# Kernel tuning notes

Measured on AMD Instinct MI355X. Metric: run time of the kernel, lower is better.

## Reference

```python
import jax
import jax.numpy as jnp
import numpy as np
from jax import lax

DIM = 48
HIDDEN = int(DIM * 2.66)  # 127, matches torch int(dim*ffn_expansion_factor)
EPS_LN = 1e-5
EPS_NORM = 1e-12


def conv2d(x, w, groups=1):
    # x: NCHW, w: OIHW, stride 1, SAME padding (all kernels here are 1x1 or 3x3 pad=1)
    return lax.conv_general_dilated(
        x, w, window_strides=(1, 1), padding='SAME',
        feature_group_count=groups,
        dimension_numbers=('NCHW', 'OIHW', 'NCHW'))


def layernorm_cbias(x, w, b):
    # Restormer WithBias_LayerNorm: normalize over channel dim (biased var)
    mu = jnp.mean(x, axis=1, keepdims=True)
    var = jnp.mean(jnp.square(x - mu), axis=1, keepdims=True)
    xn = (x - mu) * lax.rsqrt(var + EPS_LN)
    return xn * w[None, :, None, None] + b[None, :, None, None]


def l2norm_last(x):
    # torch F.normalize(dim=-1, eps=1e-12)
    n = jnp.sqrt(jnp.sum(jnp.square(x), axis=-1, keepdims=True))
    return x / jnp.maximum(n, EPS_NORM)


def setup_inputs() -> dict:
    key = jax.random.key(0)
    ks = jax.random.split(key, 16)
    s = 0.05
    B, H, W = 2, 512, 512
    return {
        'x': jax.random.normal(ks[0], (B, 3, H, W), dtype=jnp.float32),
        # OverlapPatchEmbed: Conv2d(3, 48, 3, pad=1, bias=False)
        'pe_w': jax.random.normal(ks[1], (DIM, 3, 3, 3), dtype=jnp.float32) * s,
        # norm1 (WithBias)
        'n1_w': jnp.ones((DIM,), dtype=jnp.float32),
        'n1_b': jnp.zeros((DIM,), dtype=jnp.float32),
        # MDTA attention, num_heads=1
        'temp': jnp.ones((1, 1, 1), dtype=jnp.float32),
        'qkv_w': jax.random.normal(ks[2], (DIM * 3, DIM, 1, 1), dtype=jnp.float32) * s,
        'qkv_dw_w': jax.random.normal(ks[3], (DIM * 3, 1, 3, 3), dtype=jnp.float32) * s,
        'po_w': jax.random.normal(ks[4], (DIM, DIM, 1, 1), dtype=jnp.float32) * s,
        # norm2
        'n2_w': jnp.ones((DIM,), dtype=jnp.float32),
        'n2_b': jnp.zeros((DIM,), dtype=jnp.float32),
        # GDFN
        'pi_w': jax.random.normal(ks[5], (HIDDEN * 2, DIM, 1, 1), dtype=jnp.float32) * s,
        'ffn_dw_w': jax.random.normal(ks[6], (HIDDEN * 2, 1, 3, 3), dtype=jnp.float32) * s,
        'fo_w': jax.random.normal(ks[7], (DIM, HIDDEN, 1, 1), dtype=jnp.float32) * s,
    }


def reference(x, pe_w, n1_w, n1_b, temp, qkv_w, qkv_dw_w, po_w, n2_w, n2_b, pi_w, ffn_dw_w, fo_w):
    # Patch embed
    patch = conv2d(x, pe_w)  # [B, 48, H, W]
    B, C, H, W = patch.shape

    # ---- MDTA channel attention on norm1(patch) ----
    y = layernorm_cbias(patch, n1_w, n1_b)
    qkv = conv2d(conv2d(y, qkv_w), qkv_dw_w, groups=3 * C)  # [B, 3C, H, W]
    q, k, v = jnp.split(qkv, 3, axis=1)
    # heads=1: rearrange to [B, C, H*W]
    q = l2norm_last(q.reshape(B, C, H * W))
    k = l2norm_last(k.reshape(B, C, H * W))
    v = v.reshape(B, C, H * W)
    attn = jax.nn.softmax(jnp.einsum('bcn,bdn->bcd', q, k) * temp[0, 0, 0], axis=-1)  # [B, C, C]
    out = jnp.einsum('bcd,bdn->bcn', attn, v).reshape(B, C, H, W)
    attn_out = conv2d(out, po_w)
    first = patch + attn_out

    # ---- GDFN on norm2(first) ----
    y2 = layernorm_cbias(first, n2_w, n2_b)
    h = conv2d(conv2d(y2, pi_w), ffn_dw_w, groups=2 * HIDDEN)  # [B, 254, H, W]
    x1, x2 = jnp.split(h, 2, axis=1)
    ffn = conv2d(jax.nn.gelu(x1, approximate=False) * x2, fo_w)
    return first + ffn  # second_residual [B, 48, H, W]
```

## Files before the change

### kernel.cpp

```cpp
#include <hip/hip_runtime.h>
#include <hip/hip_bf16.h>
#include <math.h>

#define HW 512
#define NPIX (HW*HW)

typedef __hip_bfloat16 bf16;
typedef __attribute__((ext_vector_type(8))) unsigned short u16x8;
typedef __attribute__((ext_vector_type(8))) short s16x8;
typedef __attribute__((ext_vector_type(4))) float f32x4;

__device__ __forceinline__ float b2f(bf16 v) { return __bfloat162float(v); }
__device__ __forceinline__ bf16 f2b(float v) { return __float2bfloat16(v); }

union fu { float f; unsigned int u; };
union bu { bf16 b; unsigned short u; };

__device__ __forceinline__ float us2f(unsigned short u) {
    fu c; c.u = ((unsigned int)u) << 16; return c.f;
}

__device__ __forceinline__ void ld_bf8(const bf16* p, float* f) {
    u16x8 u = *(const u16x8*)p;
#pragma unroll
    for (int j = 0; j < 8; j++) { fu c; c.u = ((unsigned int)u[j]) << 16; f[j] = c.f; }
}

__device__ __forceinline__ void st_bf8(bf16* p, const float* f) {
    u16x8 u;
#pragma unroll
    for (int j = 0; j < 8; j++) { bu c; c.b = f2b(f[j]); u[j] = c.u; }
    *(u16x8*)p = u;
}

__global__ __launch_bounds__(256) void k_prep(const float* __restrict__ qkvw,
                                              const float* __restrict__ piw,
                                              const float* __restrict__ fow,
                                              bf16* __restrict__ WQ,
                                              bf16* __restrict__ WP,
                                              bf16* __restrict__ WF,
                                              float* __restrict__ Z0,
                                              float* __restrict__ Z1)
{
    int idx = blockIdx.x*256 + threadIdx.x;
    if (idx < 9216) {
        int oc = idx >> 6, k = idx & 63;
        WQ[idx] = f2b(k < 48 ? qkvw[oc*48 + k] : 0.f);
    } else if (idx < 25600) {
        int j = idx - 9216; int oc = j >> 6, k = j & 63;
        WP[j] = f2b((oc < 254 && k < 48) ? piw[oc*48 + k] : 0.f);
    } else if (idx < 31744) {
        int j = idx - 25600; int oc = j >> 7, k = j & 127;
        WF[j] = f2b(k < 127 ? fow[oc*127 + k] : 0.f);
    } else if (idx < 36544) {
        int j = idx - 31744;
        if (j < 2400) Z0[j] = 0.f; else Z1[j-2400] = 0.f;
    }
}

__global__ __launch_bounds__(256) void k_pe(const float* __restrict__ x,
                                            const float* __restrict__ w,
                                            bf16* __restrict__ out)
{
    __shared__ float ws[48*27];
    for (int i = threadIdx.x; i < 48*27; i += 256) ws[i] = w[i];
    __syncthreads();
    int lane = threadIdx.x & 63, wv = threadIdx.x >> 6;
    int row = blockIdx.x*4 + wv;
    int col = lane*8;
    float a[3][3][8];
    float lf[3][3], rt[3][3];
#pragma unroll
    for (int c = 0; c < 3; c++)
#pragma unroll
        for (int r = 0; r < 3; r++) {
            int rr = row + r - 1;
            if (rr >= 0 && rr < HW) {
                const float* p = x + (size_t)c*NPIX + rr*HW + col;
                float4 u0 = *(const float4*)p, u1 = *(const float4*)(p+4);
                a[c][r][0]=u0.x; a[c][r][1]=u0.y; a[c][r][2]=u0.z; a[c][r][3]=u0.w;
                a[c][r][4]=u1.x; a[c][r][5]=u1.y; a[c][r][6]=u1.z; a[c][r][7]=u1.w;
            } else {
#pragma unroll
                for (int j = 0; j < 8; j++) a[c][r][j] = 0.f;
            }
            float l = __shfl_up(a[c][r][7], 1);  lf[c][r] = (lane==0)  ? 0.f : l;
            float rv= __shfl_down(a[c][r][0],1); rt[c][r] = (lane==63) ? 0.f : rv;
        }
    for (int oc = 0; oc < 48; oc++) {
        float acc[8];
#pragma unroll
        for (int j = 0; j < 8; j++) acc[j] = 0.f;
#pragma unroll
        for (int c = 0; c < 3; c++)
#pragma unroll
            for (int r = 0; r < 3; r++) {
                float w0 = ws[oc*27 + c*9 + r*3 + 0];
                float w1 = ws[oc*27 + c*9 + r*3 + 1];
                float w2 = ws[oc*27 + c*9 + r*3 + 2];
#pragma unroll
                for (int j = 0; j < 8; j++) {
                    float xm = (j==0) ? lf[c][r] : a[c][r][j-1];
                    float x0 = a[c][r][j];
                    float xp = (j==7) ? rt[c][r] : a[c][r][j+1];
                    acc[j] += w0*xm + w1*x0 + w2*xp;
                }
            }
        st_bf8(out + (size_t)oc*NPIX + row*HW + col, acc);
    }
}

#define YPAD 56
#define CHS 440
__global__ __launch_bounds__(256) void k_ln_dw(const bf16* __restrict__ patch,
                                               const float* __restrict__ lnw,
                                               const float* __restrict__ lnb,
                                               const s16x8* __restrict__ wq,
                                               const float* __restrict__ dww,
                                               bf16* __restrict__ outq)
{
    __shared__ unsigned short y_lds[352*YPAD];
    __shared__ unsigned short a_lds[48*CHS];
    int t = threadIdx.x;
    int c0 = blockIdx.x*32, r0 = blockIdx.y*8;

    for (int hp = t; hp < 352; hp += 256) {
        int hr = hp/34, hc = hp - hr*34;
        int gr = r0 - 1 + hr, gc = c0 - 1 + hc;
        bool ok = (hp < 340) && (gr >= 0) && (gr < HW) && (gc >= 0) && (gc < HW);
        if (ok) {
            int gpx = gr*HW + gc;
            float y[48];
            float mu = 0.f;
#pragma unroll
            for (int i = 0; i < 48; i++) { y[i] = b2f(patch[(size_t)i*NPIX + gpx]); mu += y[i]; }
            mu *= (1.f/48.f);
            float var = 0.f;
#pragma unroll
            for (int i = 0; i < 48; i++) { float d = y[i]-mu; var += d*d; }
            float s = rsqrtf(var*(1.f/48.f) + 1e-5f);
#pragma unroll
            for (int i = 0; i < 48; i++) y[i] = (y[i]-mu)*s*lnw[i] + lnb[i];
#pragma unroll
            for (int kb = 0; kb < 6; kb++) {
                union { u16x8 v; unsigned short us[8]; } pk;
#pragma unroll
                for (int j = 0; j < 8; j++) { bu b; b.b = f2b(y[kb*8+j]); pk.us[j] = b.u; }
                *(u16x8*)&y_lds[hp*YPAD + kb*8] = pk.v;
            }
        } else {
            u16x8 z = {0,0,0,0,0,0,0,0};
#pragma unroll
            for (int kb = 0; kb < 6; kb++) *(u16x8*)&y_lds[hp*YPAD + kb*8] = z;
        }
    }
    __syncthreads();

    int lane = t & 63, wv = t >> 6;
    int q = lane >> 4, n = lane & 15;
    int ch2 = lane >> 5;
    int idx5 = lane & 31;
    int orow = idx5 >> 2;
    int cg   = idx5 & 3;

#pragma unroll 1
    for (int cc = 0; cc < 3; cc++) {
        s16x8 a0[3], a1[3];
#pragma unroll
        for (int mi = 0; mi < 3; mi++) {
            int oc = (cc*3 + mi)*16 + n;
            a0[mi] = wq[oc*8 + q];
            a1[mi] = wq[oc*8 + 4 + q];
        }
#pragma unroll 1
        for (int nt = wv; nt < 22; nt += 4) {
            int hp = nt*16 + n;
            int hr = hp/34, hc = hp - hr*34;
            int abase = hr*40 + hc;
            s16x8 b0 = *(const s16x8*)&y_lds[hp*YPAD + q*8];
            s16x8 b1 = {0,0,0,0,0,0,0,0};
            if (q < 2) b1 = *(const s16x8*)&y_lds[hp*YPAD + 32 + q*8];
#pragma unroll
            for (int mi = 0; mi < 3; mi++) {
                f32x4 acc = {0.f, 0.f, 0.f, 0.f};
                acc = __builtin_amdgcn_mfma_f32_16x16x32_bf16(a0[mi], b0, acc, 0, 0, 0);
                acc = __builtin_amdgcn_mfma_f32_16x16x32_bf16(a1[mi], b1, acc, 0, 0, 0);
                int mchb = mi*16 + q*4;
#pragma unroll
                for (int r = 0; r < 4; r++) {
                    bu bb; bb.b = f2b(acc[r]);
                    a_lds[(mchb + r)*CHS + abase] = bb.u;
                }
            }
        }
        __syncthreads();

#pragma unroll 1
        for (int i = 0; i < 6; i++) {
            int chl = i*8 + wv*2 + ch2;
            int ch  = cc*48 + chl;
            float wk[9];
#pragma unroll
            for (int k = 0; k < 9; k++) wk[k] = dww[ch*9 + k];
            const unsigned short* ap = &a_lds[chl*CHS];
            float win[3][10];
#pragma unroll
            for (int kr = 0; kr < 3; kr++) {
                u16x8 A = *(const u16x8*)&ap[(orow + kr)*40 + cg*8];
                unsigned int B = *(const unsigned int*)&ap[(orow + kr)*40 + cg*8 + 8];
#pragma unroll
                for (int j = 0; j < 8; j++) win[kr][j] = us2f(A[j]);
                win[kr][8] = us2f((unsigned short)(B & 0xffffu));
                win[kr][9] = us2f((unsigned short)(B >> 16));
            }
            u16x8 pk;
#pragma unroll
            for (int j = 0; j < 8; j++) {
                float sm = 0.f;
#pragma unroll
                for (int kr = 0; kr < 3; kr++)
                    sm += wk[kr*3+0]*win[kr][j] + wk[kr*3+1]*win[kr][j+1] + wk[kr*3+2]*win[kr][j+2];
                bu b; b.b = f2b(sm); pk[j] = b.u;
            }
            *(u16x8*)&outq[(size_t)ch*NPIX + (r0 + orow)*HW + c0 + cg*8] = pk;
        }
        __syncthreads();
    }
}

template<int OC_PAD, int OC_REAL, int MT_PER_WAVE>
__global__ __launch_bounds__(256) void k_ln_mm_mfma(const bf16* __restrict__ in,
                                                    const float* __restrict__ lnw,
                                                    const float* __restrict__ lnb,
                                                    const s16x8* __restrict__ wpad,
                                                    bf16* __restrict__ out)
{
    constexpr int NMT = OC_PAD/16;
    __shared__ s16x8 y_lds[256*8];
    __shared__ unsigned short stage[OC_PAD][72];
    int t = threadIdx.x;
    int base = blockIdx.x*256;
    int px = base + t;
    float y[48];
    float mu = 0.f;
#pragma unroll
    for (int i = 0; i < 48; i++) { y[i] = b2f(in[(size_t)i*NPIX + px]); mu += y[i]; }
    mu *= (1.f/48.f);
    float var = 0.f;
#pragma unroll
    for (int i = 0; i < 48; i++) { float d = y[i]-mu; var += d*d; }
    float s = rsqrtf(var*(1.f/48.f) + 1e-5f);
#pragma unroll
    for (int i = 0; i < 48; i++) y[i] = (y[i]-mu)*s*lnw[i] + lnb[i];
#pragma unroll
    for (int kb = 0; kb < 8; kb++) {
        union { s16x8 v; unsigned short us[8]; } pk;
#pragma unroll
        for (int j = 0; j < 8; j++) {
            int c = kb*8 + j;
            bu b; b.b = f2b(c < 48 ? y[c] : 0.f);
            pk.us[j] = (c < 48) ? b.u : (unsigned short)0;
        }
        y_lds[t*8 + (kb ^ (t & 7))] = pk.v;
    }
    __syncthreads();

    int lane = t & 63, wv = t >> 6;
    int q = lane >> 4, n = lane & 15;
    s16x8 a[MT_PER_WAVE][2];
#pragma unroll
    for (int mi = 0; mi < MT_PER_WAVE; mi++) {
        int mt = wv + 4*mi;
        if (mt < NMT) {
            int oc = mt*16 + n;
            a[mi][0] = wpad[oc*8 + q];
            a[mi][1] = wpad[oc*8 + 4 + q];
        }
    }
#pragma unroll 1
    for (int g = 0; g < 4; g++) {
#pragma unroll
        for (int sub = 0; sub < 4; sub++) {
            int nt = g*4 + sub;
            int npx = nt*16 + n;
            s16x8 b0 = y_lds[npx*8 + (q ^ (npx & 7))];
            s16x8 b1 = y_lds[npx*8 + ((4 + q) ^ (npx & 7))];
#pragma unroll
            for (int mi = 0; mi < MT_PER_WAVE; mi++) {
                int mt = wv + 4*mi;
                if (mt >= NMT) continue;
                f32x4 acc = {0.f, 0.f, 0.f, 0.f};
                acc = __builtin_amdgcn_mfma_f32_16x16x32_bf16(a[mi][0], b0, acc, 0, 0, 0);
                acc = __builtin_amdgcn_mfma_f32_16x16x32_bf16(a[mi][1], b1, acc, 0, 0, 0);
                int ocb = mt*16 + q*4;
#pragma unroll
                for (int r = 0; r < 4; r++) {
                    bu bb; bb.b = f2b(acc[r]);
                    stage[ocb + r][sub*16 + n] = bb.u;
                }
            }
        }
        __syncthreads();
        if (t < OC_REAL) {
            const u16x8* sp = (const u16x8*)stage[t];
            u16x8 c0 = sp[0], c1 = sp[1], c2 = sp[2], c3 = sp[3];
            u16x8 c4 = sp[4], c5 = sp[5], c6 = sp[6], c7 = sp[7];
            u16x8* op = (u16x8*)(out + (size_t)t*NPIX + base + g*64);
            op[0] = c0; op[1] = c1; op[2] = c2; op[3] = c3;
            op[4] = c4; op[5] = c5; op[6] = c6; op[7] = c7;
        }
        __syncthreads();
    }
}

__global__ __launch_bounds__(512) void k_qkt(const bf16* __restrict__ qm,
                                             const bf16* __restrict__ km,
                                             float* __restrict__ S,
                                             float* __restrict__ sumsq)
{
    __shared__ float Sp[8][48][52];
    __shared__ float ssp[8][96];
    int t = threadIdx.x;
    int lane = t & 63, wv = t >> 6;
    int qg = lane >> 4, n = lane & 15;
    size_t px0 = (size_t)(blockIdx.x*8 + wv) * 128 + qg*8;

    f32x4 acc[3][3];
#pragma unroll
    for (int i = 0; i < 3; i++)
#pragma unroll
        for (int j = 0; j < 3; j++) acc[i][j] = (f32x4){0.f, 0.f, 0.f, 0.f};
    float sq[3] = {0.f, 0.f, 0.f}, sk[3] = {0.f, 0.f, 0.f};

#pragma unroll 2
    for (int s = 0; s < 4; s++) {
        size_t p = px0 + s*32;
        s16x8 qa[3], ka[3];
#pragma unroll
        for (int i = 0; i < 3; i++) {
            qa[i] = *(const s16x8*)&qm[(size_t)(16*i + n)*NPIX + p];
            ka[i] = *(const s16x8*)&km[(size_t)(16*i + n)*NPIX + p];
        }
#pragma unroll
        for (int i = 0; i < 3; i++)
#pragma unroll
            for (int j = 0; j < 3; j++)
                acc[i][j] = __builtin_amdgcn_mfma_f32_16x16x32_bf16(qa[i], ka[j], acc[i][j], 0, 0, 0);
#pragma unroll
        for (int i = 0; i < 3; i++) {
            union { s16x8 v; unsigned short us[8]; } uq, uk;
            uq.v = qa[i]; uk.v = ka[i];
#pragma unroll
            for (int j = 0; j < 8; j++) {
                fu cq; cq.u = ((unsigned int)uq.us[j]) << 16; sq[i] += cq.f*cq.f;
                fu ck; ck.u = ((unsigned int)uk.us[j]) << 16; sk[i] += ck.f*ck.f;
            }
        }
    }

#pragma unroll
    for (int i = 0; i < 3; i++)
#pragma unroll
        for (int j = 0; j < 3; j++)
#pragma unroll
            for (int r = 0; r < 4; r++)
                Sp[wv][16*i + qg*4 + r][16*j + n] = acc[i][j][r];
#pragma unroll
    for (int i = 0; i < 3; i++) {
        float a = sq[i], b = sk[i];
        a += __shfl_down(a, 32); a += __shfl_down(a, 16);
        b += __shfl_down(b, 32); b += __shfl_down(b, 16);
        if (lane < 16) { ssp[wv][16*i + lane] = a; ssp[wv][48 + 16*i + lane] = b; }
    }
    __syncthreads();

    for (int idx = t; idx < 2304; idx += 512) {
        int r = idx / 48, c = idx - r*48;
        float v = 0.f;
#pragma unroll
        for (int w = 0; w < 8; w++) v += Sp[w][r][c];
        atomicAdd(&S[idx], v);
    }
    if (t < 96) {
        float v = 0.f;
#pragma unroll
        for (int w = 0; w < 8; w++) v += ssp[w][t];
        atomicAdd(&sumsq[t], v);
    }
}

__global__ __launch_bounds__(256) void k_attn_final(const float* __restrict__ S,
                                                    const float* __restrict__ sumsq,
                                                    const float* __restrict__ po_w,
                                                    const float* __restrict__ temp,
                                                    float* __restrict__ M)
{
    __shared__ float attn[48][48];
    __shared__ float nrm[96];
    int t = threadIdx.x;
    if (t < 96) nrm[t] = fmaxf(sqrtf(sumsq[t]), 1e-12f);
    __syncthreads();
    float tmp = temp[0];
    if (t < 48) {
        float row[48];
        float mx = -1e30f;
#pragma unroll
        for (int d = 0; d < 48; d++) {
            float l = S[t*48+d] / (nrm[t]*nrm[48+d]) * tmp;
            row[d] = l; mx = fmaxf(mx, l);
        }
        float sum = 0.f;
#pragma unroll
        for (int d = 0; d < 48; d++) { float e = expf(row[d]-mx); sum += e; row[d] = e; }
        float inv = 1.f/sum;
#pragma unroll
        for (int d = 0; d < 48; d++) attn[t][d] = row[d]*inv;
    }
    __syncthreads();
    for (int idx = t; idx < 2304; idx += 256) {
        int cp = idx/48, d = idx%48;
        float acc = 0.f;
#pragma unroll
        for (int c = 0; c < 48; c++) acc += po_w[cp*48+c] * attn[c][d];
        M[idx] = acc;
    }
}

__global__ __launch_bounds__(256) void k_attnv(const bf16* __restrict__ v,
                                               const float* __restrict__ M,
                                               bf16* __restrict__ patch)
{
    __shared__ float Ms[48*48];
    for (int i = threadIdx.x; i < 2304; i += 256) Ms[i] = M[i];
    __syncthreads();
    int p = (blockIdx.x*256 + threadIdx.x)*2;
    float v0[48], v1[48];
#pragma unroll
    for (int i = 0; i < 48; i++) {
        unsigned int word = *(const unsigned int*)&v[(size_t)i*NPIX + p];
        fu c0, c1; c0.u = word << 16; c1.u = word & 0xffff0000u;
        v0[i] = c0.f; v1[i] = c1.f;
    }
    for (int oc = 0; oc < 48; oc++) {
        const float4* wr = (const float4*)&Ms[oc*48];
        float a0 = 0.f, a1 = 0.f;
#pragma unroll
        for (int i = 0; i < 12; i++) {
            float4 w4 = wr[i];
            a0 += w4.x*v0[4*i] + w4.y*v0[4*i+1] + w4.z*v0[4*i+2] + w4.w*v0[4*i+3];
            a1 += w4.x*v1[4*i] + w4.y*v1[4*i+1] + w4.z*v1[4*i+2] + w4.w*v1[4*i+3];
        }
        unsigned int* pp = (unsigned int*)&patch[(size_t)oc*NPIX + p];
        unsigned int old = *pp;
        fu f0, f1; f0.u = old << 16; f1.u = old & 0xffff0000u;
        bu b0, b1; b0.b = f2b(f0.f + a0); b1.b = f2b(f1.f + a1);
        *pp = (unsigned int)b0.u | ((unsigned int)b1.u << 16);
    }
}

__global__ __launch_bounds__(256) void k_dw_glu(const bf16* __restrict__ h1,
                                                const float* __restrict__ w,
                                                bf16* __restrict__ g)
{
    int ch = blockIdx.y;
    int lane = threadIdx.x & 63, wv = threadIdx.x >> 6;
    int row0 = blockIdx.x*32 + wv*8;
    int col = lane*8;
    float w1[9], w2[9];
#pragma unroll
    for (int i = 0; i < 9; i++) { w1[i] = w[ch*9+i]; w2[i] = w[(ch+127)*9+i]; }
    const bf16* i1 = h1 + (size_t)ch*NPIX;
    const bf16* i2 = h1 + (size_t)(ch+127)*NPIX;
    bf16* op = g + (size_t)ch*NPIX;
    float aa[3][8], bb[3][8];
    float lfa[3], rta[3], lfb[3], rtb[3];

    auto loadrow = [&](int s, int rr) {
        if (rr >= 0 && rr < HW) {
            ld_bf8(i1 + rr*HW + col, aa[s]);
            ld_bf8(i2 + rr*HW + col, bb[s]);
        } else {
#pragma unroll
            for (int j = 0; j < 8; j++) { aa[s][j] = 0.f; bb[s][j] = 0.f; }
        }
        float l1 = __shfl_up(aa[s][7],1);   lfa[s] = (lane==0)  ? 0.f : l1;
        float r1 = __shfl_down(aa[s][0],1); rta[s] = (lane==63) ? 0.f : r1;
        float l2 = __shfl_up(bb[s][7],1);   lfb[s] = (lane==0)  ? 0.f : l2;
        float r2 = __shfl_down(bb[s][0],1); rtb[s] = (lane==63) ? 0.f : r2;
    };
    loadrow(0, row0-1);
    loadrow(1, row0);
#pragma unroll
    for (int r = 0; r < 8; r++) {
        loadrow((r+2)%3, row0 + r + 1);
        const int s0 = r%3, s1 = (r+1)%3, s2 = (r+2)%3;
        float o[8];
#pragma unroll
        for (int j = 0; j < 8; j++) {
            float sum1 = 0.f, sum2 = 0.f;
#pragma unroll
            for (int kr = 0; kr < 3; kr++) {
                const int ss = (kr==0) ? s0 : (kr==1) ? s1 : s2;
                float xm = (j==0) ? lfa[ss] : aa[ss][j-1];
                float x0 = aa[ss][j];
                float xp = (j==7) ? rta[ss] : aa[ss][j+1];
                sum1 += w1[kr*3+0]*xm + w1[kr*3+1]*x0 + w1[kr*3+2]*xp;
                float ym = (j==0) ? lfb[ss] : bb[ss][j-1];
                float y0 = bb[ss][j];
                float yp = (j==7) ? rtb[ss] : bb[ss][j+1];
                sum2 += w2[kr*3+0]*ym + w2[kr*3+1]*y0 + w2[kr*3+2]*yp;
            }
            float ge = 0.5f*sum1*(1.f + erff(sum1*0.70710678118654752f));
            o[j] = ge*sum2;
        }
        st_bf8(op + (row0 + r)*HW + col, o);
    }
}

__global__ __launch_bounds__(256) void k_fo_mfma(const bf16* __restrict__ g,
                                                 const s16x8* __restrict__ wfo,
                                                 const bf16* __restrict__ first,
                                                 float* __restrict__ out)
{
    __shared__ s16x8 glds[256*16];
    int t = threadIdx.x;
    int base = blockIdx.x*256;
    int px = base + t;
#pragma unroll
    for (int kb = 0; kb < 16; kb++) {
        union { s16x8 v; unsigned short us[8]; } pk;
#pragma unroll
        for (int j = 0; j < 8; j++) {
            int c = kb*8 + j;
            if (c < 127) { bu b; b.b = g[(size_t)c*NPIX + px]; pk.us[j] = b.u; }
            else pk.us[j] = 0;
        }
        glds[t*16 + (kb ^ (t & 15))] = pk.v;
    }
    __syncthreads();
    int lane = t & 63, wv = t >> 6;
    int q = lane >> 4, n = lane & 15;
    s16x8 a[3][4];
#pragma unroll
    for (int mt = 0; mt < 3; mt++) {
        int oc = mt*16 + n;
#pragma unroll
        for (int kc = 0; kc < 4; kc++)
            a[mt][kc] = wfo[oc*16 + kc*4 + q];
    }
#pragma unroll 1
    for (int ni = 0; ni < 4; ni++) {
        int nt = wv*4 + ni;
        int npx = nt*16 + n;
        s16x8 b[4];
#pragma unroll
        for (int kc = 0; kc < 4; kc++)
            b[kc] = glds[npx*16 + ((kc*4 + q) ^ (npx & 15))];
        size_t pxg = base + npx;
#pragma unroll
        for (int mt = 0; mt < 3; mt++) {
            f32x4 acc = {0.f, 0.f, 0.f, 0.f};
#pragma unroll
            for (int kc = 0; kc < 4; kc++)
                acc = __builtin_amdgcn_mfma_f32_16x16x32_bf16(a[mt][kc], b[kc], acc, 0, 0, 0);
            int ocb = mt*16 + q*4;
#pragma unroll
            for (int r = 0; r < 4; r++) {
                int oc = ocb + r;
                out[(size_t)oc*NPIX + pxg] = b2f(first[(size_t)oc*NPIX + pxg]) + acc[r];
            }
        }
    }
}

extern "C" void kernel_launch(void* const* d_in, const int* in_sizes, int n_in,
                              void* d_out, int out_size, void* d_ws, size_t ws_size,
                              hipStream_t stream)
{
    const float* x     = (const float*)d_in[0];
    const float* pe_w  = (const float*)d_in[1];
    const float* n1w   = (const float*)d_in[2];
    const float* n1b   = (const float*)d_in[3];
    const float* temp  = (const float*)d_in[4];
    const float* qkvw  = (const float*)d_in[5];
    const float* qkvdw = (const float*)d_in[6];
    const float* pow_  = (const float*)d_in[7];
    const float* n2w   = (const float*)d_in[8];
    const float* n2b   = (const float*)d_in[9];
    const float* piw   = (const float*)d_in[10];
    const float* ffndw = (const float*)d_in[11];
    const float* fow   = (const float*)d_in[12];
    float* out = (float*)d_out;

    bf16*  Pb = (bf16*)d_ws;
    bf16*  A  = Pb + (size_t)48*NPIX;
    bf16*  Bq = A + (size_t)144*NPIX;
    bf16*  H1 = A;
    bf16*  G  = A + (size_t)254*NPIX;
    bf16*  WQ = A + (size_t)381*NPIX;
    bf16*  WP = WQ + 144*64;
    bf16*  WF = WP + 256*64;
    float* SM0 = (float*)(A + (size_t)384*NPIX);
    float* SM1 = SM0 + 4704;

    dim3 blk(256);
    int nb1 = NPIX/256;
    int nb2 = NPIX/512;
    int nr  = HW/4;
    int nrw = HW/32;

    k_prep<<<dim3(143), blk, 0, stream>>>(qkvw, piw, fow, WQ, WP, WF, SM0, SM1);

    for (int b = 0; b < 2; b++) {
        const float* xb   = x   + (size_t)b*3*NPIX;
        float*       outb = out + (size_t)b*48*NPIX;
        float* SMb   = b ? SM1 : SM0;
        float* sumsq = SMb;
        float* S     = SMb + 96;
        float* M     = SMb + 2400;

        k_pe<<<dim3(nr), blk, 0, stream>>>(xb, pe_w, Pb);
        k_ln_dw<<<dim3(HW/32, HW/8), blk, 0, stream>>>(Pb, n1w, n1b, (const s16x8*)WQ, qkvdw, Bq);
        k_qkt<<<dim3(NPIX/1024), dim3(512), 0, stream>>>(Bq, Bq + (size_t)48*NPIX, S, sumsq);
        k_attn_final<<<dim3(1), blk, 0, stream>>>(S, sumsq, pow_, temp, M);
        k_attnv<<<dim3(nb2), blk, 0, stream>>>(Bq + (size_t)96*NPIX, M, Pb);
        k_ln_mm_mfma<256,254,4><<<dim3(nb1), blk, 0, stream>>>(Pb, n2w, n2b, (const s16x8*)WP, H1);
        k_dw_glu<<<dim3(nrw, 127), blk, 0, stream>>>(H1, ffndw, G);
        k_fo_mfma<<<dim3(nb1), blk, 0, stream>>>(G, (const s16x8*)WF, Pb, outb);
    }
}
```

Measured before the change: 711.7 us.

## Swap MFMA operand order so accumulators hold contiguous pixels for vector stores

Swaps the A and B operands of the bf16 MFMAs in three kernels, so each lane's four accumulator values are four adjacent pixels of one channel rather than four channels of one pixel. This allows packed ushort4 stores to LDS and float4/ushort4 global loads and stores, replacing scalar 16-bit and 32-bit accesses. In the LN+depthwise kernel the halo tile is re-laid out with a 40-pixel row pitch, so MFMA pixel tiles map directly onto the padded LDS rows. That removes the hp/34 index math but computes 400 instead of 340 halo pixels, which adds some wasted MFMA work and LDS.

```diff
diff --git a/kernel.cpp b/kernel.cpp
--- a/kernel.cpp
+++ b/kernel.cpp
@@ -110,8 +110,8 @@
     }
 }
 
-#define YPAD 56
-#define CHS 440
+#define YPAD 48
+#define CHS 408
 __global__ __launch_bounds__(256) void k_ln_dw(const bf16* __restrict__ patch,
                                                const float* __restrict__ lnw,
                                                const float* __restrict__ lnb,
@@ -119,15 +119,15 @@
                                                const float* __restrict__ dww,
                                                bf16* __restrict__ outq)
 {
-    __shared__ unsigned short y_lds[352*YPAD];
+    __shared__ unsigned short y_lds[400*YPAD];
     __shared__ unsigned short a_lds[48*CHS];
     int t = threadIdx.x;
     int c0 = blockIdx.x*32, r0 = blockIdx.y*8;
 
-    for (int hp = t; hp < 352; hp += 256) {
-        int hr = hp/34, hc = hp - hr*34;
+    for (int p = t; p < 400; p += 256) {
+        int hr = p/40, hc = p - hr*40;
         int gr = r0 - 1 + hr, gc = c0 - 1 + hc;
-        bool ok = (hp < 340) && (gr >= 0) && (gr < HW) && (gc >= 0) && (gc < HW);
+        bool ok = (hc < 34) && (gr >= 0) && (gr < HW) && (gc >= 0) && (gc < HW);
         if (ok) {
             int gpx = gr*HW + gc;
             float y[48];
@@ -146,12 +146,12 @@
                 union { u16x8 v; unsigned short us[8]; } pk;
 #pragma unroll
                 for (int j = 0; j < 8; j++) { bu b; b.b = f2b(y[kb*8+j]); pk.us[j] = b.u; }
-                *(u16x8*)&y_lds[hp*YPAD + kb*8] = pk.v;
+                *(u16x8*)&y_lds[p*YPAD + kb*8] = pk.v;
             }
         } else {
             u16x8 z = {0,0,0,0,0,0,0,0};
 #pragma unroll
-            for (int kb = 0; kb < 6; kb++) *(u16x8*)&y_lds[hp*YPAD + kb*8] = z;
+            for (int kb = 0; kb < 6; kb++) *(u16x8*)&y_lds[p*YPAD + kb*8] = z;
         }
     }
     __syncthreads();
@@ -165,32 +165,28 @@
 
 #pragma unroll 1
     for (int cc = 0; cc < 3; cc++) {
-        s16x8 a0[3], a1[3];
+        s16x8 w0[3], w1[3];
 #pragma unroll
         for (int mi = 0; mi < 3; mi++) {
             int oc = (cc*3 + mi)*16 + n;
-            a0[mi] = wq[oc*8 + q];
-            a1[mi] = wq[oc*8 + 4 + q];
+            w0[mi] = wq[oc*8 + q];
+            w1[mi] = wq[oc*8 + 4 + q];
         }
 #pragma unroll 1
-        for (int nt = wv; nt < 22; nt += 4) {
-            int hp = nt*16 + n;
-            int hr = hp/34, hc = hp - hr*34;
-            int abase = hr*40 + hc;
-            s16x8 b0 = *(const s16x8*)&y_lds[hp*YPAD + q*8];
-            s16x8 b1 = {0,0,0,0,0,0,0,0};
-            if (q < 2) b1 = *(const s16x8*)&y_lds[hp*YPAD + 32 + q*8];
+        for (int nt = wv; nt < 25; nt += 4) {
+            int p16 = nt*16;
+            s16x8 ya = *(const s16x8*)&y_lds[(p16 + n)*YPAD + q*8];
+            s16x8 yb = {0,0,0,0,0,0,0,0};
+            if (q < 2) yb = *(const s16x8*)&y_lds[(p16 + n)*YPAD + 32 + q*8];
 #pragma unroll
             for (int mi = 0; mi < 3; mi++) {
                 f32x4 acc = {0.f, 0.f, 0.f, 0.f};
-                acc = __builtin_amdgcn_mfma_f32_16x16x32_bf16(a0[mi], b0, acc, 0, 0, 0);
-                acc = __builtin_amdgcn_mfma_f32_16x16x32_bf16(a1[mi], b1, acc, 0, 0, 0);
-                int mchb = mi*16 + q*4;
-#pragma unroll
-                for (int r = 0; r < 4; r++) {
-                    bu bb; bb.b = f2b(acc[r]);
-                    a_lds[(mchb + r)*CHS + abase] = bb.u;
-                }
+                acc = __builtin_amdgcn_mfma_f32_16x16x32_bf16(ya, w0[mi], acc, 0, 0, 0);
+                acc = __builtin_amdgcn_mfma_f32_16x16x32_bf16(yb, w1[mi], acc, 0, 0, 0);
+                union { unsigned short us[4]; ushort4 v; } pk;
+#pragma unroll
+                for (int r = 0; r < 4; r++) { bu bb; bb.b = f2b(acc[r]); pk.us[r] = bb.u; }
+                *(ushort4*)&a_lds[(mi*16 + n)*CHS + p16 + q*4] = pk.v;
             }
         }
         __syncthreads();
@@ -290,14 +286,13 @@
                 int mt = wv + 4*mi;
                 if (mt >= NMT) continue;
                 f32x4 acc = {0.f, 0.f, 0.f, 0.f};
-                acc = __builtin_amdgcn_mfma_f32_16x16x32_bf16(a[mi][0], b0, acc, 0, 0, 0);
-                acc = __builtin_amdgcn_mfma_f32_16x16x32_bf16(a[mi][1], b1, acc, 0, 0, 0);
-                int ocb = mt*16 + q*4;
-#pragma unroll
-                for (int r = 0; r < 4; r++) {
-                    bu bb; bb.b = f2b(acc[r]);
-                    stage[ocb + r][sub*16 + n] = bb.u;
-                }
+                acc = __builtin_amdgcn_mfma_f32_16x16x32_bf16(b0, a[mi][0], acc, 0, 0, 0);
+                acc = __builtin_amdgcn_mfma_f32_16x16x32_bf16(b1, a[mi][1], acc, 0, 0, 0);
+                int oc = mt*16 + n;
+                union { unsigned short us[4]; ushort4 v; } pk;
+#pragma unroll
+                for (int r = 0; r < 4; r++) { bu bb; bb.b = f2b(acc[r]); pk.us[r] = bb.u; }
+                *(ushort4*)&stage[oc][sub*16 + q*4] = pk.v;
             }
         }
         __syncthreads();
@@ -556,19 +551,21 @@
 #pragma unroll
         for (int kc = 0; kc < 4; kc++)
             b[kc] = glds[npx*16 + ((kc*4 + q) ^ (npx & 15))];
-        size_t pxg = base + npx;
+        size_t px4 = (size_t)base + nt*16 + q*4;
 #pragma unroll
         for (int mt = 0; mt < 3; mt++) {
             f32x4 acc = {0.f, 0.f, 0.f, 0.f};
 #pragma unroll
             for (int kc = 0; kc < 4; kc++)
-                acc = __builtin_amdgcn_mfma_f32_16x16x32_bf16(a[mt][kc], b[kc], acc, 0, 0, 0);
-            int ocb = mt*16 + q*4;
-#pragma unroll
-            for (int r = 0; r < 4; r++) {
-                int oc = ocb + r;
-                out[(size_t)oc*NPIX + pxg] = b2f(first[(size_t)oc*NPIX + pxg]) + acc[r];
-            }
+                acc = __builtin_amdgcn_mfma_f32_16x16x32_bf16(b[kc], a[mt][kc], acc, 0, 0, 0);
+            int oc = mt*16 + n;
+            ushort4 fr = *(const ushort4*)&first[(size_t)oc*NPIX + px4];
+            float4 o;
+            o.x = us2f(fr.x) + acc[0];
+            o.y = us2f(fr.y) + acc[1];
+            o.z = us2f(fr.z) + acc[2];
+            o.w = us2f(fr.w) + acc[3];
+            *(float4*)&out[(size_t)oc*NPIX + px4] = o;
         }
     }
 }
```

New measurement: 749.3 us. +5.3%, slower.
